# Performance work log

Hardware: AMD Instinct MI355X
Metric: run time of the kernel (lower is better)

## Reference

```python
import jax, jax.numpy as jnp
import numpy as np

N_NODES = 50000
N_EDGES = 500000
H = 128
C = 2


def setup_inputs() -> dict:
    key = jax.random.key(0)
    ks = jax.random.split(key, 8)
    node_repr = jax.random.normal(ks[0], (N_NODES, H), dtype=jnp.float32)
    src = jax.random.randint(ks[1], (N_EDGES,), 0, N_NODES, dtype=jnp.int32)
    dst = jax.random.randint(ks[2], (N_EDGES,), 0, N_NODES, dtype=jnp.int32)
    # Linear weights stored as (in, out); scaled like torch default init
    W1 = jax.random.normal(ks[3], (4 * H, 2 * H), dtype=jnp.float32) / np.sqrt(4 * H)
    b1 = jnp.zeros((2 * H,), dtype=jnp.float32)
    W2 = jax.random.normal(ks[4], (2 * H, H), dtype=jnp.float32) / np.sqrt(2 * H)
    b2 = jnp.zeros((H,), dtype=jnp.float32)
    W3 = jax.random.normal(ks[5], (H, C), dtype=jnp.float32) / np.sqrt(H)
    b3 = jnp.zeros((C,), dtype=jnp.float32)
    return {"node_repr": node_repr, "src": src, "dst": dst,
            "W1": W1, "b1": b1, "W2": W2, "b2": b2, "W3": W3, "b3": b3}


def reference(node_repr, src, dst, W1, b1, W2, b2, W3, b3):
    h_i = node_repr[src]                      # [E, H] gather
    h_j = node_repr[dst]                      # [E, H] gather
    diff = jnp.abs(h_i - h_j)
    product = h_i * h_j
    edge_input = jnp.concatenate([h_i, h_j, diff, product], axis=1)  # [E, 4H]
    x = jax.nn.relu(edge_input @ W1 + b1)     # [E, 2H]; dropout = identity (eval)
    x = jax.nn.relu(x @ W2 + b2)              # [E, H]
    return x @ W3 + b3                        # [E, C]
```

## Files before the change

kernel.cpp:

```cpp
#include <hip/hip_runtime.h>


#define H 128

typedef __bf16 bf16x8 __attribute__((ext_vector_type(8)));
typedef float f32x4 __attribute__((ext_vector_type(4)));

__device__ __forceinline__ unsigned short f2bf(float f) {
    unsigned u = __builtin_bit_cast(unsigned, f);
    u += 0x7FFFu + ((u >> 16) & 1u);
    return (unsigned short)(u >> 16);
}
__device__ __forceinline__ float bfhi(unsigned u) {
    return __builtin_bit_cast(float, u & 0xffff0000u);
}
__device__ __forceinline__ float bflo(unsigned u) {
    return __builtin_bit_cast(float, u << 16);
}
__device__ __forceinline__ unsigned pk2(float r0, float r1) {
    unsigned u0 = __builtin_bit_cast(unsigned, r0) + 0x8000u;
    unsigned u1 = __builtin_bit_cast(unsigned, r1) + 0x8000u;
    return __builtin_amdgcn_perm(u1, u0, 0x07060302u);
}
__device__ __forceinline__ unsigned comb(unsigned ua, unsigned ub, bool isdiff) {
    float a0 = bflo(ua), a1 = bfhi(ua);
    float b0 = bflo(ub), b1 = bfhi(ub);
    float r0 = isdiff ? fabsf(a0 - b0) : a0 * b0;
    float r1 = isdiff ? fabsf(a1 - b1) : a1 * b1;
    return pk2(r0, r1);
}
__device__ __forceinline__ unsigned short cvt1(float v) {
    unsigned u = __builtin_bit_cast(unsigned, v) + 0x8000u;
    return (unsigned short)(u >> 16);
}

__global__ void prep_node(const float* __restrict__ node, unsigned short* __restrict__ nbf) {
    int idx = blockIdx.x * 256 + threadIdx.x;
    const f32x4* p = (const f32x4*)(node) + idx;
    f32x4 v = *p;
    ushort4 w;
    w.x = f2bf(v.x); w.y = f2bf(v.y); w.z = f2bf(v.z); w.w = f2bf(v.w);
    *(ushort4*)(nbf + idx * 4) = w;
}

__global__ void prep_w1(const float* __restrict__ W1, unsigned short* __restrict__ W1P) {
    int o = blockIdx.x * 256 + threadIdx.x;
    int chunk = o >> 9;
    int g_nt = chunk >> 4;
    int ks = chunk & 15;
    int r = o & 511;
    int lane = r >> 3;
    int j = r & 7;
    int row = g_nt * 16 + (lane & 15);
    int k = ks * 32 + (lane >> 4) * 8 + j;
    W1P[o] = f2bf(W1[k * 256 + row]);
}

__global__ void prep_w2(const float* __restrict__ W2, unsigned short* __restrict__ W2P) {
    int o = blockIdx.x * 256 + threadIdx.x;
    int chunk = o >> 9;
    int g_nt = chunk >> 3;
    int ks = chunk & 7;
    int r = o & 511;
    int lane = r >> 3;
    int j = r & 7;
    int row = g_nt * 16 + (lane & 15);
    int k = ks * 32 + (lane >> 4) * 8 + j;
    W2P[o] = f2bf(W2[k * 128 + row]);
}

__launch_bounds__(256, 3)
__global__ void fused_mlp(const unsigned short* __restrict__ nbf,
                          const int* __restrict__ src,
                          const int* __restrict__ dst,
                          const unsigned short* __restrict__ W1P,
                          const float* __restrict__ b1,
                          const unsigned short* __restrict__ W2P,
                          const float* __restrict__ b2,
                          const float* __restrict__ W3,
                          const float* __restrict__ b3,
                          float* __restrict__ out,
                          int E) {
    __shared__ __align__(16) unsigned short sH[64 * 268];
    __shared__ __align__(16) float sW3[256];

    const int t = threadIdx.x;
    const int e0 = blockIdx.x * 64;

    const int lane = t & 63;
    const int wv = t >> 6;
    const int quad = lane >> 4;
    const int lrow = lane & 15;
    const int nb = wv * 64;
    const int nb2 = wv * 32;

    {
        int r = t >> 2;
        int q = t & 3;
        int e = e0 + r;
        int ec = e < E ? e : (E - 1);
        const unsigned short* hi = nbf + (long)src[ec] * H + q * 32;
        const unsigned short* hj = nbf + (long)dst[ec] * H + q * 32;
        unsigned short* rowp = sH + r * 268 + q * 32;
#pragma unroll
        for (int b = 0; b < 4; b++) {
            uint4 a = *(const uint4*)(hi + b * 8);
            uint4 c = *(const uint4*)(hj + b * 8);
            *(uint4*)(rowp + b * 8)       = a;
            *(uint4*)(rowp + 136 + b * 8) = c;
        }
        sW3[(t & 1) * 128 + (t >> 1)] = W3[t];
    }
    __syncthreads();

    const unsigned short* w1p[4];
#pragma unroll
    for (int nt = 0; nt < 4; nt++) w1p[nt] = W1P + (wv * 4 + nt) * 16 * 512 + lane * 8;

    f32x4 acc[4][4];
#pragma unroll
    for (int mt = 0; mt < 4; mt++)
#pragma unroll
        for (int nt = 0; nt < 4; nt++)
            acc[mt][nt] = (f32x4){0.f, 0.f, 0.f, 0.f};

    int aoff[4];
#pragma unroll
    for (int mt = 0; mt < 4; mt++) aoff[mt] = (mt * 16 + lrow) * 268 + quad * 8;

#pragma unroll 1
    for (int ks = 0; ks < 8; ks++) {
        const int ao = (ks < 4) ? ks * 32 : 136 + (ks - 4) * 32;
        bf16x8 bv[4], av[4];
#pragma unroll
        for (int nt = 0; nt < 4; nt++) bv[nt] = *(const bf16x8*)(w1p[nt] + ks * 512);
#pragma unroll
        for (int mt = 0; mt < 4; mt++) av[mt] = *(const bf16x8*)(sH + aoff[mt] + ao);
#pragma unroll
        for (int mt = 0; mt < 4; mt++)
#pragma unroll
            for (int nt = 0; nt < 4; nt++)
                acc[mt][nt] = __builtin_amdgcn_mfma_f32_16x16x32_bf16(av[mt], bv[nt], acc[mt][nt], 0, 0, 0);
    }

    __syncthreads();

    {
        int r = t >> 2;
        int c0 = (t & 3) * 32;
        unsigned short* rowp = sH + r * 268;
#pragma unroll
        for (int j = 0; j < 4; j++) {
            uint4 ua = *(const uint4*)(rowp + c0 + j * 8);
            uint4 ub = *(const uint4*)(rowp + 136 + c0 + j * 8);
            uint4 dd, pp;
            dd.x = comb(ua.x, ub.x, true);  dd.y = comb(ua.y, ub.y, true);
            dd.z = comb(ua.z, ub.z, true);  dd.w = comb(ua.w, ub.w, true);
            pp.x = comb(ua.x, ub.x, false); pp.y = comb(ua.y, ub.y, false);
            pp.z = comb(ua.z, ub.z, false); pp.w = comb(ua.w, ub.w, false);
            *(uint2*)(rowp + c0 + j * 8)           = (uint2){dd.x, dd.y};
            *(uint2*)(rowp + c0 + j * 8 + 4)       = (uint2){dd.z, dd.w};
            *(uint2*)(rowp + 136 + c0 + j * 8)     = (uint2){pp.x, pp.y};
            *(uint2*)(rowp + 136 + c0 + j * 8 + 4) = (uint2){pp.z, pp.w};
        }
    }
    __syncthreads();

#pragma unroll 1
    for (int ks = 0; ks < 8; ks++) {
        const int ao = (ks < 4) ? ks * 32 : 136 + (ks - 4) * 32;
        bf16x8 bv[4], av[4];
#pragma unroll
        for (int nt = 0; nt < 4; nt++) bv[nt] = *(const bf16x8*)(w1p[nt] + (ks + 8) * 512);
#pragma unroll
        for (int mt = 0; mt < 4; mt++) av[mt] = *(const bf16x8*)(sH + aoff[mt] + ao);
#pragma unroll
        for (int mt = 0; mt < 4; mt++)
#pragma unroll
            for (int nt = 0; nt < 4; nt++)
                acc[mt][nt] = __builtin_amdgcn_mfma_f32_16x16x32_bf16(av[mt], bv[nt], acc[mt][nt], 0, 0, 0);
    }

    float b1v[4];
#pragma unroll
    for (int nt = 0; nt < 4; nt++) b1v[nt] = b1[nb + nt * 16 + lrow];

    __syncthreads();
    unsigned short* sx1 = sH;
#pragma unroll
    for (int mt = 0; mt < 4; mt++)
#pragma unroll
        for (int nt = 0; nt < 4; nt++)
#pragma unroll
            for (int i = 0; i < 4; i++) {
                int row = mt * 16 + quad * 4 + i;
                int col = nb + nt * 16 + lrow;
                float v = acc[mt][nt][i] + b1v[nt];
                v = v > 0.f ? v : 0.f;
                sx1[row * 268 + col] = cvt1(v);
            }
    __syncthreads();

    const unsigned short* w2p[2];
#pragma unroll
    for (int nt = 0; nt < 2; nt++) w2p[nt] = W2P + (wv * 2 + nt) * 8 * 512 + lane * 8;

    f32x4 acc2[4][2];
#pragma unroll
    for (int mt = 0; mt < 4; mt++)
#pragma unroll
        for (int nt = 0; nt < 2; nt++)
            acc2[mt][nt] = (f32x4){0.f, 0.f, 0.f, 0.f};

#pragma unroll 1
    for (int ks = 0; ks < 8; ks++) {
        bf16x8 bv2[2], av2[4];
#pragma unroll
        for (int nt = 0; nt < 2; nt++) bv2[nt] = *(const bf16x8*)(w2p[nt] + ks * 512);
#pragma unroll
        for (int mt = 0; mt < 4; mt++) av2[mt] = *(const bf16x8*)(sx1 + aoff[mt] + ks * 32);
#pragma unroll
        for (int mt = 0; mt < 4; mt++)
#pragma unroll
            for (int nt = 0; nt < 2; nt++)
                acc2[mt][nt] = __builtin_amdgcn_mfma_f32_16x16x32_bf16(av2[mt], bv2[nt], acc2[mt][nt], 0, 0, 0);
    }

    float b2v[2];
#pragma unroll
    for (int nt = 0; nt < 2; nt++) b2v[nt] = b2[nb2 + nt * 16 + lrow];

    __syncthreads();
    unsigned short* sx2 = sH;
#pragma unroll
    for (int mt = 0; mt < 4; mt++)
#pragma unroll
        for (int nt = 0; nt < 2; nt++)
#pragma unroll
            for (int i = 0; i < 4; i++) {
                int row = mt * 16 + quad * 4 + i;
                int col = nb2 + nt * 16 + lrow;
                float v = acc2[mt][nt][i] + b2v[nt];
                v = v > 0.f ? v : 0.f;
                sx2[row * 140 + col] = cvt1(v);
            }
    __syncthreads();

    {
        int r = t >> 2;
        int c = t & 1;
        int h = (t >> 1) & 1;
        const unsigned short* xr = sx2 + r * 140 + h * 64;
        const float* w3c = sW3 + c * 128 + h * 64;
        float s = 0.f;
#pragma unroll
        for (int j = 0; j < 8; j++) {
            uint4 v = *(const uint4*)(xr + j * 8);
            const float* w = w3c + j * 8;
            s += bflo(v.x) * w[0] + bfhi(v.x) * w[1]
               + bflo(v.y) * w[2] + bfhi(v.y) * w[3]
               + bflo(v.z) * w[4] + bfhi(v.z) * w[5]
               + bflo(v.w) * w[6] + bfhi(v.w) * w[7];
        }
        s += __shfl_xor(s, 2);
        int e = e0 + r;
        if (h == 0 && e < E) out[e * 2 + c] = s + b3[c];
    }
}

extern "C" void kernel_launch(void* const* d_in, const int* in_sizes, int n_in,
                              void* d_out, int out_size, void* d_ws, size_t ws_size,
                              hipStream_t stream) {
    const float* node = (const float*)d_in[0];
    const int* src    = (const int*)d_in[1];
    const int* dst    = (const int*)d_in[2];
    const float* W1   = (const float*)d_in[3];
    const float* b1   = (const float*)d_in[4];
    const float* W2   = (const float*)d_in[5];
    const float* b2   = (const float*)d_in[6];
    const float* W3   = (const float*)d_in[7];
    const float* b3   = (const float*)d_in[8];
    float* out = (float*)d_out;
    const int NN = in_sizes[0] / H;
    const int E = in_sizes[1];

    unsigned short* W1P = (unsigned short*)d_ws;
    unsigned short* W2P = W1P + 512 * 256;
    unsigned short* NBF = W2P + 256 * 128;

    hipLaunchKernelGGL(prep_node, dim3((NN * H / 4 + 255) / 256), dim3(256), 0, stream, node, NBF);
    hipLaunchKernelGGL(prep_w1, dim3(512), dim3(256), 0, stream, W1, W1P);
    hipLaunchKernelGGL(prep_w2, dim3(128), dim3(256), 0, stream, W2, W2P);
    const int nblk = (E + 63) / 64;
    hipLaunchKernelGGL(fused_mlp, dim3(nblk), dim3(256), 0, stream,
                       NBF, src, dst, W1P, b1, W2P, b2, W3, b3, out, E);
}
```

Baseline: 382.6 us.

## Double-buffer weight tiles in LDS via async global_load_lds prefetch

Replaces direct per-iteration global loads of packed W1/W2 fragments with asynchronous global-to-LDS DMA into per-wave double buffers. Each k-step's weights are prefetched two steps ahead, and waitcnt gates consumption, so load latency overlaps the MFMA work. The extra 32KB of LDS leads to launch bounds being lowered from 3 to 2 blocks per CU, which cuts occupancy. Correctness relies on the vmcnt counting, which also covers the gathered node loads issued around the prefetches.

```diff
diff --git a/kernel.cpp b/kernel.cpp
--- a/kernel.cpp
+++ b/kernel.cpp
@@ -5,6 +5,19 @@
 
 typedef __bf16 bf16x8 __attribute__((ext_vector_type(8)));
 typedef float f32x4 __attribute__((ext_vector_type(4)));
+
+typedef __attribute__((address_space(1))) const unsigned int gu32;
+typedef __attribute__((address_space(3))) unsigned int lu32;
+
+__device__ __forceinline__ void dma16(const unsigned short* g, unsigned short* ldsBase) {
+    __builtin_amdgcn_global_load_lds((gu32*)g, (lu32*)ldsBase, 16, 0, 0);
+}
+template <int N>
+__device__ __forceinline__ void wait_vm() {
+    __builtin_amdgcn_s_waitcnt(0xF70 | N);
+    asm volatile("" ::: "memory");
+}
+__device__ __forceinline__ void membar() { asm volatile("" ::: "memory"); }
 
 __device__ __forceinline__ unsigned short f2bf(float f) {
     unsigned u = __builtin_bit_cast(unsigned, f);
@@ -69,7 +82,7 @@
     W2P[o] = f2bf(W2[k * 128 + row]);
 }
 
-__launch_bounds__(256, 3)
+__launch_bounds__(256, 2)
 __global__ void fused_mlp(const unsigned short* __restrict__ nbf,
                           const int* __restrict__ src,
                           const int* __restrict__ dst,
@@ -82,6 +95,7 @@
                           float* __restrict__ out,
                           int E) {
     __shared__ __align__(16) unsigned short sH[64 * 268];
+    __shared__ __align__(16) unsigned short sB[2][4][2048];
     __shared__ __align__(16) float sW3[256];
 
     const int t = threadIdx.x;
@@ -93,6 +107,16 @@
     const int lrow = lane & 15;
     const int nb = wv * 64;
     const int nb2 = wv * 32;
+
+    const unsigned short* w1g = W1P + (wv * 4) * 16 * 512 + lane * 8;
+    const unsigned short* w2g = W2P + (wv * 2) * 8 * 512 + lane * 8;
+    unsigned short* sBw0 = &sB[0][wv][0];
+    unsigned short* sBw1 = &sB[1][wv][0];
+
+#pragma unroll
+    for (int nt = 0; nt < 4; nt++) dma16(w1g + nt * 8192, sBw0 + nt * 512);
+#pragma unroll
+    for (int nt = 0; nt < 4; nt++) dma16(w1g + nt * 8192 + 512, sBw1 + nt * 512);
 
     {
         int r = t >> 2;
@@ -113,10 +137,6 @@
     }
     __syncthreads();
 
-    const unsigned short* w1p[4];
-#pragma unroll
-    for (int nt = 0; nt < 4; nt++) w1p[nt] = W1P + (wv * 4 + nt) * 16 * 512 + lane * 8;
-
     f32x4 acc[4][4];
 #pragma unroll
     for (int mt = 0; mt < 4; mt++)
@@ -130,10 +150,12 @@
 
 #pragma unroll 1
     for (int ks = 0; ks < 8; ks++) {
+        if (ks == 7) wait_vm<0>(); else wait_vm<4>();
+        const unsigned short* bb = (ks & 1) ? sBw1 : sBw0;
         const int ao = (ks < 4) ? ks * 32 : 136 + (ks - 4) * 32;
         bf16x8 bv[4], av[4];
 #pragma unroll
-        for (int nt = 0; nt < 4; nt++) bv[nt] = *(const bf16x8*)(w1p[nt] + ks * 512);
+        for (int nt = 0; nt < 4; nt++) bv[nt] = *(const bf16x8*)(bb + nt * 512 + lane * 8);
 #pragma unroll
         for (int mt = 0; mt < 4; mt++) av[mt] = *(const bf16x8*)(sH + aoff[mt] + ao);
 #pragma unroll
@@ -141,7 +163,19 @@
 #pragma unroll
             for (int nt = 0; nt < 4; nt++)
                 acc[mt][nt] = __builtin_amdgcn_mfma_f32_16x16x32_bf16(av[mt], bv[nt], acc[mt][nt], 0, 0, 0);
-    }
+        if (ks < 6) {
+            membar();
+            unsigned short* db = (ks & 1) ? sBw1 : sBw0;
+#pragma unroll
+            for (int nt = 0; nt < 4; nt++)
+                dma16(w1g + nt * 8192 + (ks + 2) * 512, db + nt * 512);
+        }
+    }
+
+#pragma unroll
+    for (int nt = 0; nt < 4; nt++) dma16(w1g + nt * 8192 + 8 * 512, sBw0 + nt * 512);
+#pragma unroll
+    for (int nt = 0; nt < 4; nt++) dma16(w1g + nt * 8192 + 9 * 512, sBw1 + nt * 512);
 
     __syncthreads();
 
@@ -168,10 +202,12 @@
 
 #pragma unroll 1
     for (int ks = 0; ks < 8; ks++) {
+        if (ks == 7) wait_vm<0>(); else wait_vm<4>();
+        const unsigned short* bb = (ks & 1) ? sBw1 : sBw0;
         const int ao = (ks < 4) ? ks * 32 : 136 + (ks - 4) * 32;
         bf16x8 bv[4], av[4];
 #pragma unroll
-        for (int nt = 0; nt < 4; nt++) bv[nt] = *(const bf16x8*)(w1p[nt] + (ks + 8) * 512);
+        for (int nt = 0; nt < 4; nt++) bv[nt] = *(const bf16x8*)(bb + nt * 512 + lane * 8);
 #pragma unroll
         for (int mt = 0; mt < 4; mt++) av[mt] = *(const bf16x8*)(sH + aoff[mt] + ao);
 #pragma unroll
@@ -179,11 +215,23 @@
 #pragma unroll
             for (int nt = 0; nt < 4; nt++)
                 acc[mt][nt] = __builtin_amdgcn_mfma_f32_16x16x32_bf16(av[mt], bv[nt], acc[mt][nt], 0, 0, 0);
+        if (ks < 6) {
+            membar();
+            unsigned short* db = (ks & 1) ? sBw1 : sBw0;
+#pragma unroll
+            for (int nt = 0; nt < 4; nt++)
+                dma16(w1g + nt * 8192 + (ks + 10) * 512, db + nt * 512);
+        }
     }
 
     float b1v[4];
 #pragma unroll
     for (int nt = 0; nt < 4; nt++) b1v[nt] = b1[nb + nt * 16 + lrow];
+    membar();
+#pragma unroll
+    for (int nt = 0; nt < 2; nt++) dma16(w2g + nt * 4096, sBw0 + nt * 512);
+#pragma unroll
+    for (int nt = 0; nt < 2; nt++) dma16(w2g + nt * 4096 + 512, sBw1 + nt * 512);
 
     __syncthreads();
     unsigned short* sx1 = sH;
@@ -201,10 +249,6 @@
             }
     __syncthreads();
 
-    const unsigned short* w2p[2];
-#pragma unroll
-    for (int nt = 0; nt < 2; nt++) w2p[nt] = W2P + (wv * 2 + nt) * 8 * 512 + lane * 8;
-
     f32x4 acc2[4][2];
 #pragma unroll
     for (int mt = 0; mt < 4; mt++)
@@ -214,9 +258,11 @@
 
 #pragma unroll 1
     for (int ks = 0; ks < 8; ks++) {
+        if (ks == 7) wait_vm<0>(); else wait_vm<2>();
+        const unsigned short* bb = (ks & 1) ? sBw1 : sBw0;
         bf16x8 bv2[2], av2[4];
 #pragma unroll
-        for (int nt = 0; nt < 2; nt++) bv2[nt] = *(const bf16x8*)(w2p[nt] + ks * 512);
+        for (int nt = 0; nt < 2; nt++) bv2[nt] = *(const bf16x8*)(bb + nt * 512 + lane * 8);
 #pragma unroll
         for (int mt = 0; mt < 4; mt++) av2[mt] = *(const bf16x8*)(sx1 + aoff[mt] + ks * 32);
 #pragma unroll
@@ -224,6 +270,13 @@
 #pragma unroll
             for (int nt = 0; nt < 2; nt++)
                 acc2[mt][nt] = __builtin_amdgcn_mfma_f32_16x16x32_bf16(av2[mt], bv2[nt], acc2[mt][nt], 0, 0, 0);
+        if (ks < 6) {
+            membar();
+            unsigned short* db = (ks & 1) ? sBw1 : sBw0;
+#pragma unroll
+            for (int nt = 0; nt < 2; nt++)
+                dma16(w2g + nt * 4096 + (ks + 2) * 512, db + nt * 512);
+        }
     }
 
     float b2v[2];
```

New measurement: 452.0 us. 1.18x slower.

## Persistent 512-thread blocks holding W1/W2 fragments in registers across edge tiles

Applied to the files above, without the earlier changes.

The fused MLP becomes a persistent kernel: 256 blocks of 512 threads (8 waves) loop over 64-edge tiles. Each wave loads its slice of W1 (32 output columns over all K) and W2 (16 columns) into registers once, so the per-tile global weight reloads go away. Gather, combine and output work are redistributed over 512 threads. In exchange, register pressure is very high (about 192 VGPRs of weight fragments), and the grid of only 256 blocks may underfill the GPU or cause spills, while the single sH buffer still serializes gather and compute within each block.

```diff
diff --git a/kernel.cpp b/kernel.cpp
--- a/kernel.cpp
+++ b/kernel.cpp
@@ -69,7 +69,7 @@
     W2P[o] = f2bf(W2[k * 128 + row]);
 }
 
-__launch_bounds__(256, 3)
+__launch_bounds__(512, 2)
 __global__ void fused_mlp(const unsigned short* __restrict__ nbf,
                           const int* __restrict__ src,
                           const int* __restrict__ dst,
@@ -80,191 +80,176 @@
                           const float* __restrict__ W3,
                           const float* __restrict__ b3,
                           float* __restrict__ out,
-                          int E) {
+                          int E, int nTiles) {
     __shared__ __align__(16) unsigned short sH[64 * 268];
     __shared__ __align__(16) float sW3[256];
 
     const int t = threadIdx.x;
-    const int e0 = blockIdx.x * 64;
-
     const int lane = t & 63;
     const int wv = t >> 6;
     const int quad = lane >> 4;
     const int lrow = lane & 15;
-    const int nb = wv * 64;
-    const int nb2 = wv * 32;
-
-    {
-        int r = t >> 2;
-        int q = t & 3;
-        int e = e0 + r;
-        int ec = e < E ? e : (E - 1);
-        const unsigned short* hi = nbf + (long)src[ec] * H + q * 32;
-        const unsigned short* hj = nbf + (long)dst[ec] * H + q * 32;
-        unsigned short* rowp = sH + r * 268 + q * 32;
-#pragma unroll
-        for (int b = 0; b < 4; b++) {
-            uint4 a = *(const uint4*)(hi + b * 8);
-            uint4 c = *(const uint4*)(hj + b * 8);
-            *(uint4*)(rowp + b * 8)       = a;
-            *(uint4*)(rowp + 136 + b * 8) = c;
-        }
-        sW3[(t & 1) * 128 + (t >> 1)] = W3[t];
-    }
-    __syncthreads();
-
-    const unsigned short* w1p[4];
-#pragma unroll
-    for (int nt = 0; nt < 4; nt++) w1p[nt] = W1P + (wv * 4 + nt) * 16 * 512 + lane * 8;
-
-    f32x4 acc[4][4];
-#pragma unroll
-    for (int mt = 0; mt < 4; mt++)
-#pragma unroll
-        for (int nt = 0; nt < 4; nt++)
-            acc[mt][nt] = (f32x4){0.f, 0.f, 0.f, 0.f};
+    const int nb = wv * 32;
+    const int nb2 = wv * 16;
+
+    if (t < 256) sW3[(t & 1) * 128 + (t >> 1)] = W3[t];
+
+    float b1v[2];
+#pragma unroll
+    for (int nt = 0; nt < 2; nt++) b1v[nt] = b1[nb + nt * 16 + lrow];
+    const float b2v = b2[nb2 + lrow];
+
+    bf16x8 bres1[16][2];
+#pragma unroll
+    for (int ks = 0; ks < 16; ks++)
+#pragma unroll
+        for (int j = 0; j < 2; j++)
+            bres1[ks][j] = *(const bf16x8*)(W1P + ((2 * wv + j) * 16 + ks) * 512 + lane * 8);
+    bf16x8 bres2[8];
+#pragma unroll
+    for (int ks = 0; ks < 8; ks++)
+        bres2[ks] = *(const bf16x8*)(W2P + (wv * 8 + ks) * 512 + lane * 8);
 
     int aoff[4];
 #pragma unroll
     for (int mt = 0; mt < 4; mt++) aoff[mt] = (mt * 16 + lrow) * 268 + quad * 8;
 
-#pragma unroll 1
-    for (int ks = 0; ks < 8; ks++) {
-        const int ao = (ks < 4) ? ks * 32 : 136 + (ks - 4) * 32;
-        bf16x8 bv[4], av[4];
-#pragma unroll
-        for (int nt = 0; nt < 4; nt++) bv[nt] = *(const bf16x8*)(w1p[nt] + ks * 512);
-#pragma unroll
-        for (int mt = 0; mt < 4; mt++) av[mt] = *(const bf16x8*)(sH + aoff[mt] + ao);
+    for (int tile = blockIdx.x; tile < nTiles; tile += gridDim.x) {
+        const int e0 = tile * 64;
+        __syncthreads();
+
+        {
+            int r = t >> 3;
+            int side = (t >> 2) & 1;
+            int q = t & 3;
+            int e = e0 + r;
+            int ec = e < E ? e : (E - 1);
+            int nid = side ? dst[ec] : src[ec];
+            const unsigned short* g = nbf + (long)nid * H + q * 32;
+            unsigned short* rowp = sH + r * 268 + (side ? 136 : 0) + q * 32;
+#pragma unroll
+            for (int b = 0; b < 4; b++)
+                *(uint4*)(rowp + b * 8) = *(const uint4*)(g + b * 8);
+        }
+        __syncthreads();
+
+        f32x4 acc[4][2];
 #pragma unroll
         for (int mt = 0; mt < 4; mt++)
 #pragma unroll
-            for (int nt = 0; nt < 4; nt++)
-                acc[mt][nt] = __builtin_amdgcn_mfma_f32_16x16x32_bf16(av[mt], bv[nt], acc[mt][nt], 0, 0, 0);
-    }
-
-    __syncthreads();
-
-    {
-        int r = t >> 2;
-        int c0 = (t & 3) * 32;
-        unsigned short* rowp = sH + r * 268;
-#pragma unroll
-        for (int j = 0; j < 4; j++) {
-            uint4 ua = *(const uint4*)(rowp + c0 + j * 8);
-            uint4 ub = *(const uint4*)(rowp + 136 + c0 + j * 8);
-            uint4 dd, pp;
-            dd.x = comb(ua.x, ub.x, true);  dd.y = comb(ua.y, ub.y, true);
-            dd.z = comb(ua.z, ub.z, true);  dd.w = comb(ua.w, ub.w, true);
-            pp.x = comb(ua.x, ub.x, false); pp.y = comb(ua.y, ub.y, false);
-            pp.z = comb(ua.z, ub.z, false); pp.w = comb(ua.w, ub.w, false);
-            *(uint2*)(rowp + c0 + j * 8)           = (uint2){dd.x, dd.y};
-            *(uint2*)(rowp + c0 + j * 8 + 4)       = (uint2){dd.z, dd.w};
-            *(uint2*)(rowp + 136 + c0 + j * 8)     = (uint2){pp.x, pp.y};
-            *(uint2*)(rowp + 136 + c0 + j * 8 + 4) = (uint2){pp.z, pp.w};
-        }
-    }
-    __syncthreads();
-
-#pragma unroll 1
-    for (int ks = 0; ks < 8; ks++) {
-        const int ao = (ks < 4) ? ks * 32 : 136 + (ks - 4) * 32;
-        bf16x8 bv[4], av[4];
-#pragma unroll
-        for (int nt = 0; nt < 4; nt++) bv[nt] = *(const bf16x8*)(w1p[nt] + (ks + 8) * 512);
-#pragma unroll
-        for (int mt = 0; mt < 4; mt++) av[mt] = *(const bf16x8*)(sH + aoff[mt] + ao);
+            for (int nt = 0; nt < 2; nt++)
+                acc[mt][nt] = (f32x4){0.f, 0.f, 0.f, 0.f};
+
+#pragma unroll
+        for (int ks = 0; ks < 8; ks++) {
+            const int ao = (ks < 4) ? ks * 32 : 136 + (ks - 4) * 32;
+            bf16x8 av[4];
+#pragma unroll
+            for (int mt = 0; mt < 4; mt++) av[mt] = *(const bf16x8*)(sH + aoff[mt] + ao);
+#pragma unroll
+            for (int mt = 0; mt < 4; mt++)
+#pragma unroll
+                for (int nt = 0; nt < 2; nt++)
+                    acc[mt][nt] = __builtin_amdgcn_mfma_f32_16x16x32_bf16(av[mt], bres1[ks][nt], acc[mt][nt], 0, 0, 0);
+        }
+        __syncthreads();
+
+        {
+            int r = t >> 3;
+            int c0 = (t & 7) * 16;
+            unsigned short* rowp = sH + r * 268;
+#pragma unroll
+            for (int j = 0; j < 2; j++) {
+                uint4 ua = *(const uint4*)(rowp + c0 + j * 8);
+                uint4 ub = *(const uint4*)(rowp + 136 + c0 + j * 8);
+                uint4 dd, pp;
+                dd.x = comb(ua.x, ub.x, true);  dd.y = comb(ua.y, ub.y, true);
+                dd.z = comb(ua.z, ub.z, true);  dd.w = comb(ua.w, ub.w, true);
+                pp.x = comb(ua.x, ub.x, false); pp.y = comb(ua.y, ub.y, false);
+                pp.z = comb(ua.z, ub.z, false); pp.w = comb(ua.w, ub.w, false);
+                *(uint4*)(rowp + c0 + j * 8)       = dd;
+                *(uint4*)(rowp + 136 + c0 + j * 8) = pp;
+            }
+        }
+        __syncthreads();
+
+#pragma unroll
+        for (int ks = 0; ks < 8; ks++) {
+            const int ao = (ks < 4) ? ks * 32 : 136 + (ks - 4) * 32;
+            bf16x8 av[4];
+#pragma unroll
+            for (int mt = 0; mt < 4; mt++) av[mt] = *(const bf16x8*)(sH + aoff[mt] + ao);
+#pragma unroll
+            for (int mt = 0; mt < 4; mt++)
+#pragma unroll
+                for (int nt = 0; nt < 2; nt++)
+                    acc[mt][nt] = __builtin_amdgcn_mfma_f32_16x16x32_bf16(av[mt], bres1[ks + 8][nt], acc[mt][nt], 0, 0, 0);
+        }
+        __syncthreads();
+
+        unsigned short* sx1 = sH;
 #pragma unroll
         for (int mt = 0; mt < 4; mt++)
 #pragma unroll
-            for (int nt = 0; nt < 4; nt++)
-                acc[mt][nt] = __builtin_amdgcn_mfma_f32_16x16x32_bf16(av[mt], bv[nt], acc[mt][nt], 0, 0, 0);
-    }
-
-    float b1v[4];
-#pragma unroll
-    for (int nt = 0; nt < 4; nt++) b1v[nt] = b1[nb + nt * 16 + lrow];
-
-    __syncthreads();
-    unsigned short* sx1 = sH;
-#pragma unroll
-    for (int mt = 0; mt < 4; mt++)
-#pragma unroll
-        for (int nt = 0; nt < 4; nt++)
+            for (int nt = 0; nt < 2; nt++)
+#pragma unroll
+                for (int i = 0; i < 4; i++) {
+                    int row = mt * 16 + quad * 4 + i;
+                    int col = nb + nt * 16 + lrow;
+                    float v = acc[mt][nt][i] + b1v[nt];
+                    v = v > 0.f ? v : 0.f;
+                    sx1[row * 268 + col] = cvt1(v);
+                }
+        __syncthreads();
+
+        f32x4 acc2[4];
+#pragma unroll
+        for (int mt = 0; mt < 4; mt++) acc2[mt] = (f32x4){0.f, 0.f, 0.f, 0.f};
+#pragma unroll
+        for (int ks = 0; ks < 8; ks++) {
+            bf16x8 av2[4];
+#pragma unroll
+            for (int mt = 0; mt < 4; mt++) av2[mt] = *(const bf16x8*)(sx1 + aoff[mt] + ks * 32);
+#pragma unroll
+            for (int mt = 0; mt < 4; mt++)
+                acc2[mt] = __builtin_amdgcn_mfma_f32_16x16x32_bf16(av2[mt], bres2[ks], acc2[mt], 0, 0, 0);
+        }
+        __syncthreads();
+
+        unsigned short* sx2 = sH;
+#pragma unroll
+        for (int mt = 0; mt < 4; mt++)
 #pragma unroll
             for (int i = 0; i < 4; i++) {
                 int row = mt * 16 + quad * 4 + i;
-                int col = nb + nt * 16 + lrow;
-                float v = acc[mt][nt][i] + b1v[nt];
-                v = v > 0.f ? v : 0.f;
-                sx1[row * 268 + col] = cvt1(v);
-            }
-    __syncthreads();
-
-    const unsigned short* w2p[2];
-#pragma unroll
-    for (int nt = 0; nt < 2; nt++) w2p[nt] = W2P + (wv * 2 + nt) * 8 * 512 + lane * 8;
-
-    f32x4 acc2[4][2];
-#pragma unroll
-    for (int mt = 0; mt < 4; mt++)
-#pragma unroll
-        for (int nt = 0; nt < 2; nt++)
-            acc2[mt][nt] = (f32x4){0.f, 0.f, 0.f, 0.f};
-
-#pragma unroll 1
-    for (int ks = 0; ks < 8; ks++) {
-        bf16x8 bv2[2], av2[4];
-#pragma unroll
-        for (int nt = 0; nt < 2; nt++) bv2[nt] = *(const bf16x8*)(w2p[nt] + ks * 512);
-#pragma unroll
-        for (int mt = 0; mt < 4; mt++) av2[mt] = *(const bf16x8*)(sx1 + aoff[mt] + ks * 32);
-#pragma unroll
-        for (int mt = 0; mt < 4; mt++)
-#pragma unroll
-            for (int nt = 0; nt < 2; nt++)
-                acc2[mt][nt] = __builtin_amdgcn_mfma_f32_16x16x32_bf16(av2[mt], bv2[nt], acc2[mt][nt], 0, 0, 0);
-    }
-
-    float b2v[2];
-#pragma unroll
-    for (int nt = 0; nt < 2; nt++) b2v[nt] = b2[nb2 + nt * 16 + lrow];
-
-    __syncthreads();
-    unsigned short* sx2 = sH;
-#pragma unroll
-    for (int mt = 0; mt < 4; mt++)
-#pragma unroll
-        for (int nt = 0; nt < 2; nt++)
-#pragma unroll
-            for (int i = 0; i < 4; i++) {
-                int row = mt * 16 + quad * 4 + i;
-                int col = nb2 + nt * 16 + lrow;
-                float v = acc2[mt][nt][i] + b2v[nt];
+                int col = nb2 + lrow;
+                float v = acc2[mt][i] + b2v;
                 v = v > 0.f ? v : 0.f;
                 sx2[row * 140 + col] = cvt1(v);
             }
-    __syncthreads();
-
-    {
-        int r = t >> 2;
-        int c = t & 1;
-        int h = (t >> 1) & 1;
-        const unsigned short* xr = sx2 + r * 140 + h * 64;
-        const float* w3c = sW3 + c * 128 + h * 64;
-        float s = 0.f;
-#pragma unroll
-        for (int j = 0; j < 8; j++) {
-            uint4 v = *(const uint4*)(xr + j * 8);
-            const float* w = w3c + j * 8;
-            s += bflo(v.x) * w[0] + bfhi(v.x) * w[1]
-               + bflo(v.y) * w[2] + bfhi(v.y) * w[3]
-               + bflo(v.z) * w[4] + bfhi(v.z) * w[5]
-               + bflo(v.w) * w[6] + bfhi(v.w) * w[7];
-        }
-        s += __shfl_xor(s, 2);
-        int e = e0 + r;
-        if (h == 0 && e < E) out[e * 2 + c] = s + b3[c];
+        __syncthreads();
+
+        {
+            int r = t >> 3;
+            int c = (t >> 2) & 1;
+            int h = t & 3;
+            const unsigned short* xr = sx2 + r * 140 + h * 32;
+            const float* w3c = sW3 + c * 128 + h * 32;
+            float s = 0.f;
+#pragma unroll
+            for (int j = 0; j < 4; j++) {
+                uint4 v = *(const uint4*)(xr + j * 8);
+                const float* w = w3c + j * 8;
+                s += bflo(v.x) * w[0] + bfhi(v.x) * w[1]
+                   + bflo(v.y) * w[2] + bfhi(v.y) * w[3]
+                   + bflo(v.z) * w[4] + bfhi(v.z) * w[5]
+                   + bflo(v.w) * w[6] + bfhi(v.w) * w[7];
+            }
+            s += __shfl_xor(s, 1);
+            s += __shfl_xor(s, 2);
+            int e = e0 + r;
+            if (h == 0 && e < E) out[e * 2 + c] = s + b3[c];
+        }
     }
 }
 
@@ -291,7 +276,7 @@
     hipLaunchKernelGGL(prep_node, dim3((NN * H / 4 + 255) / 256), dim3(256), 0, stream, node, NBF);
     hipLaunchKernelGGL(prep_w1, dim3(512), dim3(256), 0, stream, W1, W1P);
     hipLaunchKernelGGL(prep_w2, dim3(128), dim3(256), 0, stream, W2, W2P);
-    const int nblk = (E + 63) / 64;
-    hipLaunchKernelGGL(fused_mlp, dim3(nblk), dim3(256), 0, stream,
-                       NBF, src, dst, W1P, b1, W2P, b2, W3, b3, out, E);
-}
+    const int nTiles = (E + 63) / 64;
+    hipLaunchKernelGGL(fused_mlp, dim3(256), dim3(512), 0, stream,
+                       NBF, src, dst, W1P, b1, W2P, b2, W3, b3, out, E, nTiles);
+}
```

After: 549.7 us. 1.44x slower.
